# Performance work log

Hardware: AMD Instinct MI355X
Metric: run time of the kernel (lower is better)

Reference implementation:

```python
import jax, jax.numpy as jnp
import numpy as np


def setup_inputs() -> dict:
    key = jax.random.key(0)
    ks = jax.random.split(key, 7)
    B, F, D = 1024, 32, 64
    H = [128, 128, 128]
    x = jax.random.normal(ks[0], (B, F, D), dtype=jnp.float32)
    # Conv1d(k=1) weights: (out, in) where in = prev_field * F, Kaiming-ish scale
    W0 = jax.random.normal(ks[1], (H[0], F * F), dtype=jnp.float32) * 0.02
    b0 = jnp.zeros((H[0],), dtype=jnp.float32)
    W1 = jax.random.normal(ks[2], (H[1], H[0] * F), dtype=jnp.float32) * 0.02
    b1 = jnp.zeros((H[1],), dtype=jnp.float32)
    W2 = jax.random.normal(ks[3], (H[2], H[1] * F), dtype=jnp.float32) * 0.02
    b2 = jnp.zeros((H[2],), dtype=jnp.float32)
    return {"x": x, "W0": W0, "b0": b0, "W1": W1, "b1": b1, "W2": W2, "b2": b2}


def reference(x, W0, b0, W1, b1, W2, b2):
    # CIN: per layer, outer product of current hidden with base fields along
    # embed dim, then 1x1 conv (channel mix) + ReLU. We fuse the bhmd
    # intermediate directly into the contraction: W reshaped to (o, h, m)
    # matches torch's reshape(b, h*m, d) channel ordering (h major, m minor).
    F = x.shape[1]
    x0 = x  # (b, m=F, d)
    h = x
    res = []
    for W, b in ((W0, b0), (W1, b1), (W2, b2)):
        o = W.shape[0]
        Wr = W.reshape(o, h.shape[1], F)  # (o, h, m)
        z = jnp.einsum('bhd,bmd,ohm->bod', h, x0, Wr) + b[None, :, None]
        h = jax.nn.relu(z)
        res.append(h)
    out = jnp.concatenate(res, axis=1)  # (b, sum(H), d)
    return jnp.sum(out, axis=-1)  # (b, sum(H))
```

## Files before the change

kernel.cpp:

```cpp
#include <hip/hip_runtime.h>
#include <stdint.h>


typedef __attribute__((ext_vector_type(8))) _Float16 f16x8;
typedef __attribute__((ext_vector_type(2))) _Float16 f16x2;
typedef __attribute__((ext_vector_type(4))) float f32x4;
typedef __attribute__((ext_vector_type(16))) float f32x16;
typedef __attribute__((ext_vector_type(4))) int i32x4;
typedef __attribute__((ext_vector_type(2))) int i32x2;

union AB {
  i32x4 i;
  f16x8 h;
  uint32_t u[4];
};
union AB2 {
  i32x2 i;
  uint32_t u[2];
};

static __device__ __forceinline__ uint32_t pkmul(uint32_t a, uint32_t b) {
  f16x2 r = __builtin_bit_cast(f16x2, a) * __builtin_bit_cast(f16x2, b);
  return __builtin_bit_cast(uint32_t, r);
}
static __device__ __forceinline__ uint32_t pkcvt(float a, float b) {
  return __builtin_bit_cast(uint32_t, __builtin_amdgcn_cvt_pkrtz(a, b));
}
static __device__ __forceinline__ void gload_lds16(const void* g, void* l) {
  __builtin_amdgcn_global_load_lds(
      (const __attribute__((address_space(1))) void*)g,
      (__attribute__((address_space(3))) void*)l, 16, 0, 0);
}

#define HP 140

__global__ __launch_bounds__(512, 4) void cin_main(
    const float* __restrict__ x, const uint16_t* __restrict__ wp,
    const float* __restrict__ bias0, const float* __restrict__ bias1,
    const float* __restrict__ bias2, float* __restrict__ out) {
  __shared__ __align__(16) uint16_t hT[2][64][HP];
  __shared__ __align__(16) uint16_t wtile[2][16][512];
  __shared__ float psum[2][2][128];

  const int tid = threadIdx.x;
  const int w = tid >> 6, lane = tid & 63;
  const int ot = w & 3;
  const int g = w >> 2;
  const int hi = lane >> 5;
  const int l31 = lane & 31;
  const int lane8 = lane * 8;
  const int bb = blockIdx.x * 2;

  for (int e = tid; e < 4096; e += 512) {
    int p = e >> 11, m = (e >> 6) & 31, d = e & 63;
    hT[p][d][m] =
        __builtin_bit_cast(uint16_t, (_Float16)x[(size_t)(bb + p) * 2048 + m * 64 + d]);
  }
  __syncthreads();

  const int drow = g * 32 + l31;

  AB xf[2][2];
#pragma unroll
  for (int b2 = 0; b2 < 2; ++b2)
#pragma unroll
    for (int s = 0; s < 2; ++s) {
      AB2 lo = *(const AB2*)&hT[b2][drow][s * 16 + hi * 8];
      AB2 hi4 = *(const AB2*)&hT[b2][drow][s * 16 + hi * 8 + 4];
      xf[b2][s].u[0] = lo.u[0];
      xf[b2][s].u[1] = lo.u[1];
      xf[b2][s].u[2] = hi4.u[0];
      xf[b2][s].u[3] = hi4.u[1];
    }

  f32x16 acc[2];

  const int fi0 = 2 * w, fi1 = 2 * w + 1;

#pragma unroll
  for (int L = 0; L < 3; ++L) {
    const int Kch = (L == 0) ? 32 : 128;
    const uint16_t* wl = (L == 0) ? wp : (L == 1) ? wp + 131072 : wp + 655360;
    const float* bias = (L == 0) ? bias0 : (L == 1) ? bias1 : bias2;
    const int T = Kch >> 1;

    const uint16_t* s0 = wl +
        ((size_t)((fi0 >> 2) * Kch + ((fi0 >> 1) & 1)) << 10) +
        ((fi0 & 1) << 9) + lane8;
    const uint16_t* s1 = wl +
        ((size_t)((fi1 >> 2) * Kch + ((fi1 >> 1) & 1)) << 10) +
        ((fi1 & 1) << 9) + lane8;

#pragma unroll
    for (int b2 = 0; b2 < 2; ++b2)
#pragma unroll
      for (int r = 0; r < 16; ++r) acc[b2][r] = 0.f;

    auto stage = [&](int p, int c) {
      gload_lds16(s0 + ((size_t)c << 10), &wtile[p][fi0][0]);
      gload_lds16(s1 + ((size_t)c << 10), &wtile[p][fi1][0]);
    };
    auto tileCompute = [&](int p, int c) {
      uint32_t hv0 = *(const uint32_t*)&hT[0][drow][c];
      uint32_t hv1 = *(const uint32_t*)&hT[1][drow][c];
#pragma unroll
      for (int cc = 0; cc < 2; ++cc) {
        uint32_t hd0 = __builtin_amdgcn_perm(hv0, hv0,
                                             cc ? 0x03020302u : 0x01000100u);
        uint32_t hd1 = __builtin_amdgcn_perm(hv1, hv1,
                                             cc ? 0x03020302u : 0x01000100u);
#pragma unroll
        for (int s = 0; s < 2; ++s) {
          AB wf;
          wf.i = *(const i32x4*)&wtile[p][(ot << 2) | (cc << 1) | s][lane8];
          AB bf0, bf1;
#pragma unroll
          for (int k = 0; k < 4; ++k) {
            bf0.u[k] = pkmul(hd0, xf[0][s].u[k]);
            bf1.u[k] = pkmul(hd1, xf[1][s].u[k]);
          }
          acc[0] = __builtin_amdgcn_mfma_f32_32x32x16_f16(wf.h, bf0.h,
                                                          acc[0], 0, 0, 0);
          acc[1] = __builtin_amdgcn_mfma_f32_32x32x16_f16(wf.h, bf1.h,
                                                          acc[1], 0, 0, 0);
        }
      }
    };

    stage(0, 0);
    __syncthreads();
#pragma unroll 1
    for (int t = 0; t < T; ++t) {
      const int p = t & 1;
      if (t + 1 < T) stage(p ^ 1, 2 * (t + 1));
      tileCompute(p, 2 * t);
      __syncthreads();
    }

#pragma unroll
    for (int rg = 0; rg < 4; ++rg) {
      f32x4 bv = *(const f32x4*)(bias + ot * 32 + 8 * rg + 4 * hi);
#pragma unroll
      for (int b2 = 0; b2 < 2; ++b2)
#pragma unroll
        for (int rr = 0; rr < 4; ++rr)
          acc[b2][4 * rg + rr] = fmaxf(acc[b2][4 * rg + rr] + bv[rr], 0.f);
    }

    if (L < 2) {
#pragma unroll
      for (int b2 = 0; b2 < 2; ++b2)
#pragma unroll
        for (int rg = 0; rg < 4; ++rg) {
          uint2 pk;
          pk.x = pkcvt(acc[b2][4 * rg + 0], acc[b2][4 * rg + 1]);
          pk.y = pkcvt(acc[b2][4 * rg + 2], acc[b2][4 * rg + 3]);
          *(uint2*)&hT[b2][drow][ot * 32 + 8 * rg + 4 * hi] = pk;
        }
    }

#pragma unroll
    for (int b2 = 0; b2 < 2; ++b2)
#pragma unroll
      for (int rg = 0; rg < 4; ++rg)
#pragma unroll
        for (int rr = 0; rr < 4; ++rr) {
          float s = acc[b2][4 * rg + rr];
          s += __shfl_xor(s, 1);
          s += __shfl_xor(s, 2);
          s += __shfl_xor(s, 4);
          s += __shfl_xor(s, 8);
          s += __shfl_xor(s, 16);
          if (l31 == 0) psum[g][b2][ot * 32 + 8 * rg + 4 * hi + rr] = s;
        }
    __syncthreads();
    if (tid < 256) {
      int p2 = tid >> 7, o = tid & 127;
      out[(size_t)(bb + p2) * 384 + L * 128 + o] =
          psum[0][p2][o] + psum[1][p2][o];
    }
  }
}

__global__ void pack_w_all(const float* __restrict__ W0, const float* __restrict__ W1,
                           const float* __restrict__ W2, uint16_t* __restrict__ Wp) {
  int blk = blockIdx.x;
  const float* W;
  uint16_t* dst;
  int kshift;
  if (blk < 64)       { W = W0; dst = Wp;          kshift = 5; }
  else if (blk < 320) { W = W1; dst = Wp + 131072; kshift = 7; blk -= 64; }
  else                { W = W2; dst = Wp + 655360; kshift = 7; blk -= 320; }
  int idx = blk * 256 + threadIdx.x;
  int Kq = 1 << (kshift + 2);
  int o = idx >> (kshift + 2);
  int kq = idx & (Kq - 1);
  int c = kq >> 2, s = (kq >> 1) & 1, hi = kq & 1;
  int ot = o >> 5, li = o & 31;
  const float* src = W + ((size_t)o << (kshift + 5)) + kq * 8;
  uint4 val;
  val.x = pkcvt(src[0], src[1]);
  val.y = pkcvt(src[2], src[3]);
  val.z = pkcvt(src[4], src[5]);
  val.w = pkcvt(src[6], src[7]);
  size_t d16 = ((((size_t)(ot << kshift) + c) * 2 + s) << 9) + (hi << 8) + (li << 3);
  *(uint4*)(dst + d16) = val;
}

extern "C" void kernel_launch(void* const* d_in, const int* in_sizes, int n_in,
                              void* d_out, int out_size, void* d_ws, size_t ws_size,
                              hipStream_t stream) {
  (void)in_sizes; (void)n_in; (void)out_size; (void)ws_size;
  const float* x  = (const float*)d_in[0];
  const float* W0 = (const float*)d_in[1];
  const float* b0 = (const float*)d_in[2];
  const float* W1 = (const float*)d_in[3];
  const float* b1 = (const float*)d_in[4];
  const float* W2 = (const float*)d_in[5];
  const float* b2 = (const float*)d_in[6];
  uint16_t* wpacked = (uint16_t*)d_ws;

  hipLaunchKernelGGL(pack_w_all, dim3(576), dim3(256), 0, stream, W0, W1, W2, wpacked);
  hipLaunchKernelGGL(cin_main, dim3(512), dim3(512), 0, stream,
                     x, wpacked, b0, b1, b2, (float*)d_out);
}
```

Measured before the change: 217.8 us.

## Load weight fragments directly from global into registers, drop LDS staging

```diff
diff --git a/kernel.cpp b/kernel.cpp
--- a/kernel.cpp
+++ b/kernel.cpp
@@ -26,11 +26,6 @@
 static __device__ __forceinline__ uint32_t pkcvt(float a, float b) {
   return __builtin_bit_cast(uint32_t, __builtin_amdgcn_cvt_pkrtz(a, b));
 }
-static __device__ __forceinline__ void gload_lds16(const void* g, void* l) {
-  __builtin_amdgcn_global_load_lds(
-      (const __attribute__((address_space(1))) void*)g,
-      (__attribute__((address_space(3))) void*)l, 16, 0, 0);
-}
 
 #define HP 140
 
@@ -39,7 +34,6 @@
     const float* __restrict__ bias0, const float* __restrict__ bias1,
     const float* __restrict__ bias2, float* __restrict__ out) {
   __shared__ __align__(16) uint16_t hT[2][64][HP];
-  __shared__ __align__(16) uint16_t wtile[2][16][512];
   __shared__ float psum[2][2][128];
 
   const int tid = threadIdx.x;
@@ -75,67 +69,77 @@
 
   f32x16 acc[2];
 
-  const int fi0 = 2 * w, fi1 = 2 * w + 1;
-
 #pragma unroll
   for (int L = 0; L < 3; ++L) {
     const int Kch = (L == 0) ? 32 : 128;
     const uint16_t* wl = (L == 0) ? wp : (L == 1) ? wp + 131072 : wp + 655360;
     const float* bias = (L == 0) ? bias0 : (L == 1) ? bias1 : bias2;
-    const int T = Kch >> 1;
-
-    const uint16_t* s0 = wl +
-        ((size_t)((fi0 >> 2) * Kch + ((fi0 >> 1) & 1)) << 10) +
-        ((fi0 & 1) << 9) + lane8;
-    const uint16_t* s1 = wl +
-        ((size_t)((fi1 >> 2) * Kch + ((fi1 >> 1) & 1)) << 10) +
-        ((fi1 & 1) << 9) + lane8;
+
+    const uint16_t* pb =
+        wl + ((size_t)__builtin_amdgcn_readfirstlane(ot * Kch) << 10);
 
 #pragma unroll
     for (int b2 = 0; b2 < 2; ++b2)
 #pragma unroll
       for (int r = 0; r < 16; ++r) acc[b2][r] = 0.f;
 
-    auto stage = [&](int p, int c) {
-      gload_lds16(s0 + ((size_t)c << 10), &wtile[p][fi0][0]);
-      gload_lds16(s1 + ((size_t)c << 10), &wtile[p][fi1][0]);
+    AB wbuf[2][2][2];
+    uint32_t hvA[2], hvB[2];
+
+    auto loadSlot = [&](int sl, int c) {
+#pragma unroll
+      for (int cc = 0; cc < 2; ++cc)
+#pragma unroll
+        for (int s = 0; s < 2; ++s)
+          wbuf[sl][cc][s].i =
+              *(const i32x4*)(pb + ((c + cc) << 10) + (s << 9) + lane8);
     };
-    auto tileCompute = [&](int p, int c) {
-      uint32_t hv0 = *(const uint32_t*)&hT[0][drow][c];
-      uint32_t hv1 = *(const uint32_t*)&hT[1][drow][c];
+    auto loadHv = [&](uint32_t (&hv)[2], int c) {
+#pragma unroll
+      for (int b2 = 0; b2 < 2; ++b2)
+        hv[b2] = *(const uint32_t*)&hT[b2][drow][c];
+    };
+    auto computeStep = [&](const AB (&wb)[2][2], const uint32_t (&hv)[2]) {
 #pragma unroll
       for (int cc = 0; cc < 2; ++cc) {
-        uint32_t hd0 = __builtin_amdgcn_perm(hv0, hv0,
+        uint32_t hd0 = __builtin_amdgcn_perm(hv[0], hv[0],
                                              cc ? 0x03020302u : 0x01000100u);
-        uint32_t hd1 = __builtin_amdgcn_perm(hv1, hv1,
+        uint32_t hd1 = __builtin_amdgcn_perm(hv[1], hv[1],
                                              cc ? 0x03020302u : 0x01000100u);
 #pragma unroll
         for (int s = 0; s < 2; ++s) {
-          AB wf;
-          wf.i = *(const i32x4*)&wtile[p][(ot << 2) | (cc << 1) | s][lane8];
           AB bf0, bf1;
 #pragma unroll
           for (int k = 0; k < 4; ++k) {
             bf0.u[k] = pkmul(hd0, xf[0][s].u[k]);
             bf1.u[k] = pkmul(hd1, xf[1][s].u[k]);
           }
-          acc[0] = __builtin_amdgcn_mfma_f32_32x32x16_f16(wf.h, bf0.h,
+          acc[0] = __builtin_amdgcn_mfma_f32_32x32x16_f16(wb[cc][s].h, bf0.h,
                                                           acc[0], 0, 0, 0);
-          acc[1] = __builtin_amdgcn_mfma_f32_32x32x16_f16(wf.h, bf1.h,
+          acc[1] = __builtin_amdgcn_mfma_f32_32x32x16_f16(wb[cc][s].h, bf1.h,
                                                           acc[1], 0, 0, 0);
         }
       }
     };
 
-    stage(0, 0);
-    __syncthreads();
+    loadSlot(0, 0);
+    loadSlot(1, 2);
+    loadHv(hvA, 0);
+
 #pragma unroll 1
-    for (int t = 0; t < T; ++t) {
-      const int p = t & 1;
-      if (t + 1 < T) stage(p ^ 1, 2 * (t + 1));
-      tileCompute(p, 2 * t);
-      __syncthreads();
-    }
+    for (int c0 = 0; c0 < Kch - 4; c0 += 4) {
+      loadHv(hvB, c0 + 2);
+      computeStep(wbuf[0], hvA);
+      loadSlot(0, c0 + 4);
+      __builtin_amdgcn_sched_barrier(0);
+      loadHv(hvA, c0 + 4);
+      computeStep(wbuf[1], hvB);
+      loadSlot(1, c0 + 6);
+      __builtin_amdgcn_sched_barrier(0);
+    }
+    loadHv(hvB, Kch - 2);
+    computeStep(wbuf[0], hvA);
+    computeStep(wbuf[1], hvB);
 
 #pragma unroll
     for (int rg = 0; rg < 4; ++rg) {
@@ -146,6 +150,8 @@
         for (int rr = 0; rr < 4; ++rr)
           acc[b2][4 * rg + rr] = fmaxf(acc[b2][4 * rg + rr] + bv[rr], 0.f);
     }
+
+    __syncthreads();
 
     if (L < 2) {
 #pragma unroll
```

Result: slower. 226.9 us (+4.2%).
